# Performance work log

Hardware: AMD Instinct MI355X
Metric: run time of the kernel (lower is better)

## Reference

```python
import jax, jax.numpy as jnp
import numpy as np
from jax import lax

L = 2        # encoder layers
D = 256      # d_model
H = 8        # nhead
DH = D // H  # head dim
CF = 2       # compression_factor (default in CustomizedAttn)
FF = 2048    # dim_feedforward
B = 10       # batch (forced: null_k has shape (10,1,D))
HH = 40
WW = 40
T = HH * WW  # seq len = 1600
EPS = 1e-5


def setup_inputs() -> dict:
    key = jax.random.key(0)
    ks = jax.random.split(key, 16)
    f = lambda k, shp: jax.random.normal(k, shp, jnp.float32) * 0.02
    return {
        "src": jax.random.normal(ks[0], (B, D, HH, WW), jnp.float32),
        "pos_embed": jax.random.normal(ks[1], (B, D, HH, WW), jnp.float32),
        "Wq": f(ks[2], (L, D, D)),
        "Wk": f(ks[3], (L, D, D)),
        "Wv": f(ks[4], (L, D, D)),
        "Wo": f(ks[5], (L, D, D)),
        "bo": jnp.zeros((L, D), jnp.float32),
        "conv_w": f(ks[6], (L, D, D // H, CF)),  # grouped Conv1d weight [out, in/groups, k]
        "conv_b": jnp.zeros((L, D), jnp.float32),
        "null_k": f(ks[7], (L, B, 1, D)),
        "null_v": f(ks[8], (L, B, 1, D)),
        "ln1_g": jnp.ones((L, D), jnp.float32),
        "ln1_b": jnp.zeros((L, D), jnp.float32),
        "ln2_g": jnp.ones((L, D), jnp.float32),
        "ln2_b": jnp.zeros((L, D), jnp.float32),
        "W1": f(ks[9], (L, FF, D)),
        "b1": jnp.zeros((L, FF), jnp.float32),
        "W2": f(ks[10], (L, D, FF)),
        "b2": jnp.zeros((L, D), jnp.float32),
    }


def _layernorm(x, g, b):
    m = jnp.mean(x, axis=-1, keepdims=True)
    v = jnp.var(x, axis=-1, keepdims=True)
    return (x - m) * lax.rsqrt(v + EPS) * g + b


def _attn(x, pos, Wq, Wk, Wv, Wo, bo, cw, cb, nk, nv):
    # x, pos: [B, T, D]
    qk = x + pos
    q = qk @ Wq.T
    k = qk @ Wk.T
    v = x @ Wv.T
    # torch: padding = cf - t % cf -> always in [1, cf], so padding ALWAYS applied
    pad = CF - (T % CF)
    k = jnp.pad(k, ((0, 0), (pad, 0), (0, 0)))
    v = jnp.pad(v, ((0, 0), (pad, 0), (0, 0)))

    def compress(t_):  # grouped strided Conv1d over time, shared weights for k and v
        y = lax.conv_general_dilated(
            t_.transpose(0, 2, 1), cw, (CF,), "VALID",
            dimension_numbers=("NCH", "OIH", "NCH"), feature_group_count=H)
        return (y + cb[None, :, None]).transpose(0, 2, 1)

    k = jnp.concatenate([nk, compress(k)], axis=1)  # [B, Tc+10, D]
    v = jnp.concatenate([nv, compress(v)], axis=1)
    split = lambda t_: t_.reshape(B, t_.shape[1], H, DH).transpose(0, 2, 1, 3)
    qh, kh, vh = split(q), split(k), split(v)
    # NOTE: scale uses FULL d_model (d ** -0.5), faithful to the source.
    dots = jnp.einsum("bhid,bhjd->bhij", qh, kh) * (D ** -0.5)
    # NOTE: the source computes softmax(dots) but then overwrites it with
    # dropout(dots); at inference attention weights are the raw scaled dots.
    out = jnp.einsum("bhij,bhjd->bhid", dots, vh)
    out = out.transpose(0, 2, 1, 3).reshape(B, T, D)
    return out @ Wo.T + bo


def reference(src, pos_embed, Wq, Wk, Wv, Wo, bo, conv_w, conv_b, null_k, null_v,
              ln1_g, ln1_b, ln2_g, ln2_b, W1, b1, W2, b2):
    x = src.reshape(B, D, T).transpose(0, 2, 1)        # [B, T, D]
    pos = pos_embed.reshape(B, D, T).transpose(0, 2, 1)
    for l in range(L):
        a = _attn(x, pos, Wq[l], Wk[l], Wv[l], Wo[l], bo[l],
                  conv_w[l], conv_b[l], null_k[l], null_v[l])
        x = _layernorm(x + a, ln1_g[l], ln1_b[l])
        ff = jnp.maximum(x @ W1[l].T + b1[l], 0.0) @ W2[l].T + b2[l]
        x = _layernorm(x + ff, ln2_g[l], ln2_b[l])
    return x.transpose(0, 2, 1).reshape(B, D, HH, WW)
```

## Files before the change

### kernel.cpp

```cpp
#include <hip/hip_runtime.h>
#include <math.h>

typedef __attribute__((ext_vector_type(8))) short short8;
typedef __attribute__((ext_vector_type(4))) short short4v;
typedef __attribute__((ext_vector_type(4))) float f32x4;
typedef unsigned int u32;

constexpr int Bsz = 10;
constexpr int Dm  = 256;
constexpr int Hh  = 8;
constexpr int Tt  = 1600;
constexpr int FFd = 2048;
constexpr int Tkv = 802;
constexpr int JCH = 8;
constexpr size_t Fsz  = (size_t)Bsz * Tt * Dm;
constexpr size_t PAD  = 65536;
constexpr size_t KVsz = (size_t)Bsz * Tkv * Dm;
constexpr size_t FHsz = (size_t)Bsz * Tt * FFd;
constexpr size_t WBsz = 2621440;

__device__ float g_x[Fsz];
__device__ float g_qk[Fsz];
__device__ float g_t[Fsz];
__device__ float g_kc[KVsz];
__device__ float g_vc[KVsz];
__device__ float g_kvm[(size_t)Bsz * Hh * 32 * 32];
__device__ float g_kvp[(size_t)JCH * Bsz * Hh * 32 * 32];
__device__ float g_pos[Fsz];
__device__ unsigned short g_xb[Fsz + PAD];
__device__ unsigned short g_qkb[Fsz + PAD];
__device__ unsigned short g_tb[Fsz + PAD];
__device__ unsigned short g_qb[Fsz + PAD];
__device__ __attribute__((aligned(16))) unsigned short g_ffh[FHsz + PAD];
__device__ unsigned short g_wb[WBsz];
__device__ unsigned short g_wo2[(size_t)Bsz * Dm * Dm];

__device__ __forceinline__ float* selbuf(int id) {
  switch (id) {
    case 0: return g_x;
    case 1: return g_qk;
    case 2: return g_t;
    case 3: return g_kc;
    case 4: return g_vc;
    case 5: return g_kvm;
    case 6: return (float*)g_ffh;
    default: return (float*)g_ffh + Fsz;
  }
}
__device__ __forceinline__ unsigned short* selbufb(int id) {
  switch (id) {
    case 0: return g_xb;
    case 1: return g_qkb;
    case 2: return g_tb;
    case 3: return g_ffh;
    default: return g_qb;
  }
}

__device__ __forceinline__ unsigned short f2b(float x) {
  unsigned int u = __float_as_uint(x);
  u += 0x7FFFu + ((u >> 16) & 1u);
  return (unsigned short)(u >> 16);
}
__device__ __forceinline__ float b2f(unsigned short u) {
  return __uint_as_float(((unsigned int)u) << 16);
}

__global__ __launch_bounds__(256) void wconv_all_k(
    const float* __restrict__ Wk, const float* __restrict__ Wq,
    const float* __restrict__ Wv, const float* __restrict__ Wo,
    const float* __restrict__ W1, const float* __restrict__ W2) {
  const int i = blockIdx.x * 256 + threadIdx.x;
  float v;
  if (i < 262144) {
    const int l = i >> 17, r = i & 131071;
    v = (r < 65536) ? Wk[l * 65536 + r] : Wq[l * 65536 + (r - 65536)];
  } else if (i < 393216) {
    v = Wv[i - 262144];
  } else if (i < 524288) {
    v = Wo[i - 393216];
  } else if (i < 1572864) {
    v = W1[i - 524288];
  } else {
    v = W2[i - 1572864];
  }
  g_wb[i] = f2b(v);
}

__global__ __launch_bounds__(256) void trans_in2_k(const float* __restrict__ src,
                                                   const float* __restrict__ pose) {
  __shared__ float ts[32][33];
  __shared__ float tp[32][33];
  const int tx = threadIdx.x & 31, ty = threadIdx.x >> 5;
  const int t0 = blockIdx.x * 32, d0 = blockIdx.y * 32, b = blockIdx.z;
  #pragma unroll
  for (int i = ty; i < 32; i += 8) {
    const size_t gi = ((size_t)(b * Dm + d0 + i)) * Tt + t0 + tx;
    ts[i][tx] = src[gi];
    tp[i][tx] = pose[gi];
  }
  __syncthreads();
  #pragma unroll
  for (int i = ty; i < 32; i += 8) {
    const size_t idx = ((size_t)(b * Tt + t0 + i)) * Dm + d0 + tx;
    const float s = ts[tx][i], p = tp[tx][i];
    g_x[idx] = s;
    g_pos[idx] = p;
    g_xb[idx] = f2b(s);
    g_qkb[idx] = f2b(s + p);
  }
}

__global__ __launch_bounds__(256) void trans_out_k(float* out) {
  __shared__ float tile[32][33];
  const int tx = threadIdx.x & 31, ty = threadIdx.x >> 5;
  const int t0 = blockIdx.x * 32, d0 = blockIdx.y * 32, b = blockIdx.z;
  #pragma unroll
  for (int i = ty; i < 32; i += 8)
    tile[i][tx] = g_x[((size_t)(b * Tt + t0 + i)) * Dm + d0 + tx];
  __syncthreads();
  #pragma unroll
  for (int i = ty; i < 32; i += 8)
    out[((size_t)(b * Dm + d0 + i)) * Tt + t0 + tx] = tile[tx][i];
}

template<int BN, bool DUAL, bool PERB, bool RELU, bool BIAS, bool CBF16>
__global__ __launch_bounds__(256) void gemm2_k(
    int Aid, int woff, const float* __restrict__ bias, int Cid, int C2id,
    int NB, int M, int N, int K) {
  constexpr int BM = 128, BK = 64;
  constexpr int ACH = BM * 8;
  constexpr int BCH = BN * 8;
  constexpr int NW = BN / 32;
  __shared__ short8 As8[3][ACH];
  __shared__ short8 Bs8[3][BCH];
  const int tid = threadIdx.x;
  const int lane = tid & 63, wid = tid >> 6;
  const int wr = wid >> 1, wc = wid & 1;

  const int nwg = gridDim.x;
  const int bid = blockIdx.x;
  const int q = nwg >> 3, r = nwg & 7;
  const int xcd = bid & 7, seq = bid >> 3;
  const int wgid = (xcd < r ? xcd * (q + 1) : r * (q + 1) + (xcd - r) * q) + seq;

  int m0, n0, mlim;
  const unsigned short* W16;
  if constexpr (PERB) {
    const int per = 13 * NB;
    const int b = wgid / per;
    const int rem = wgid - b * per;
    m0 = b * Tt + (rem / NB) * BM;
    n0 = (rem % NB) * BN;
    mlim = b * Tt + Tt;
    W16 = g_wo2 + (size_t)b * 65536;
  } else {
    m0 = (wgid / NB) * BM;
    n0 = (wgid % NB) * BN;
    mlim = M;
    W16 = g_wb + woff;
  }

  const unsigned short* A16 = selbufb(Aid);
  const bool second = DUAL && (n0 >= 256);
  float* Cf = selbuf(second ? C2id : Cid);
  unsigned short* C16 = selbufb(second ? C2id : Cid);
  const int gn0 = second ? n0 - 256 : n0;
  const int cstride = DUAL ? 256 : N;

  f32x4 acc[4][NW];
  #pragma unroll
  for (int m = 0; m < 4; ++m)
    #pragma unroll
    for (int n = 0; n < NW; ++n) acc[m][n] = (f32x4){0.f, 0.f, 0.f, 0.f};

  const int lkc = lane >> 4, lrc = lane & 15;

  auto stage = [&](int t, int buf) {
    const int k0 = t * BK;
    #pragma unroll
    for (int i = 0; i < ACH / 256; ++i) {
      const int c = tid + i * 256;
      const int row = c >> 3, kc = c & 7;
      const unsigned short* gs = A16 + (size_t)(m0 + row) * K + k0 +
                                 ((kc ^ (row & 7)) << 3);
      __builtin_amdgcn_global_load_lds(
          (const __attribute__((address_space(1))) u32*)gs,
          (__attribute__((address_space(3))) u32*)&As8[buf][c], 16, 0, 0);
    }
    #pragma unroll
    for (int i = 0; i < BCH / 256; ++i) {
      const int c = tid + i * 256;
      const int row = c >> 3, kc = c & 7;
      const unsigned short* gs = W16 + (size_t)(n0 + row) * K + k0 +
                                 ((kc ^ (row & 7)) << 3);
      __builtin_amdgcn_global_load_lds(
          (const __attribute__((address_space(1))) u32*)gs,
          (__attribute__((address_space(3))) u32*)&Bs8[buf][c], 16, 0, 0);
    }
  };

  const int nt = K / BK;
  stage(0, 0);
  if (nt > 1) stage(1, 1);
  int cur = 0, nxt = 2;
  for (int t = 0; t < nt; ++t) {
    if (t + 1 < nt) {
      asm volatile("s_waitcnt vmcnt(6)" ::: "memory");
    } else {
      asm volatile("s_waitcnt vmcnt(0)" ::: "memory");
    }
    __builtin_amdgcn_sched_barrier(0);
    __builtin_amdgcn_s_barrier();
    __builtin_amdgcn_sched_barrier(0);
    if (t + 2 < nt) stage(t + 2, nxt);
    #pragma unroll
    for (int kk = 0; kk < 2; ++kk) {
      short8 af[4], bf[NW];
      #pragma unroll
      for (int m = 0; m < 4; ++m) {
        const int r2 = wr * 64 + m * 16 + lrc;
        af[m] = As8[cur][r2 * 8 + ((kk * 4 + lkc) ^ (r2 & 7))];
      }
      #pragma unroll
      for (int n = 0; n < NW; ++n) {
        const int cn = wc * (BN / 2) + n * 16 + lrc;
        bf[n] = Bs8[cur][cn * 8 + ((kk * 4 + lkc) ^ (cn & 7))];
      }
      #pragma unroll
      for (int m = 0; m < 4; ++m)
        #pragma unroll
        for (int n = 0; n < NW; ++n)
          acc[m][n] = __builtin_amdgcn_mfma_f32_16x16x32_bf16(
              af[m], bf[n], acc[m][n], 0, 0, 0);
    }
    cur = (cur == 2) ? 0 : cur + 1;
    nxt = (nxt == 2) ? 0 : nxt + 1;
  }

  constexpr int CSTR = (BN == 64) ? BN + 4 : BN;
  float* ldsC = (float*)&As8[0][0];
  {
    asm volatile("s_waitcnt vmcnt(0)" ::: "memory");
    __builtin_amdgcn_s_barrier();
    const int r0 = lkc * 4;
    #pragma unroll
    for (int m = 0; m < 4; ++m)
      #pragma unroll
      for (int n = 0; n < NW; ++n) {
        const int col = wc * (BN / 2) + n * 16 + lrc;
        #pragma unroll
        for (int j = 0; j < 4; ++j)
          ldsC[(wr * 64 + m * 16 + r0 + j) * CSTR + col] = acc[m][n][j];
      }
    __syncthreads();
  }
  if constexpr (CBF16) {
    constexpr int CH = BM * BN / 8;
    #pragma unroll
    for (int i = 0; i < CH / 256; ++i) {
      const int c = tid + i * 256;
      const int rowl = c / (BN / 8), col8 = (c % (BN / 8)) * 8;
      if (PERB && m0 + rowl >= mlim) continue;
      short8 v;
      #pragma unroll
      for (int j = 0; j < 8; ++j) {
        float x = ldsC[rowl * CSTR + col8 + j];
        if (BIAS) x += bias[gn0 + col8 + j];
        if (RELU) x = fmaxf(x, 0.f);
        v[j] = (short)f2b(x);
      }
      *(short8*)(C16 + (size_t)(m0 + rowl) * cstride + gn0 + col8) = v;
    }
  } else {
    constexpr int CH = BM * BN / 4;
    #pragma unroll
    for (int i = 0; i < CH / 256; ++i) {
      const int c = tid + i * 256;
      const int rowl = c / (BN / 4), col4 = (c % (BN / 4)) * 4;
      if (PERB && m0 + rowl >= mlim) continue;
      float4 v;
      float* pv = &v.x;
      #pragma unroll
      for (int j = 0; j < 4; ++j) {
        float x = ldsC[rowl * CSTR + col4 + j];
        if (BIAS) x += bias[gn0 + col4 + j];
        if (RELU) x = fmaxf(x, 0.f);
        pv[j] = x;
      }
      *(float4*)(Cf + (size_t)(m0 + rowl) * cstride + gn0 + col4) = v;
    }
  }
}

__global__ __launch_bounds__(1024, 1) void gemmf_k(
    int Aid, int w1off, int w2off, const float* __restrict__ b1p,
    const float* __restrict__ b2p) {
  constexpr int BM = 128, NCH = 32;
  __shared__ short8 ws[4096];
  __shared__ short8 h8[512];
  __shared__ float b1f[1024];
  const int tid = threadIdx.x;
  const int lane = tid & 63, wid = tid >> 6;
  const int lkc = lane >> 4, lrc = lane & 15;
  const int nwg = gridDim.x, bid = blockIdx.x;
  const int q = nwg >> 3, r = nwg & 7;
  const int xcd = bid & 7, seq = bid >> 3;
  const int wgid = (xcd < r ? xcd * (q + 1) : r * (q + 1) + (xcd - r) * q) + seq;
  const int half = (wgid >= 125) ? 1 : 0;
  const int m0 = (wgid - half * 125) * BM;
  const int hb = half * 1024;
  const unsigned short* A16 = selbufb(Aid);
  const unsigned short* W1p = g_wb + w1off;
  const unsigned short* W2p = g_wb + w2off;
  float* Cf = half ? g_t : g_qk;

  #pragma unroll
  for (int i = 0; i < 4; ++i) {
    const int c = tid + i * 1024;
    const int row = c >> 5, kc = c & 31;
    const unsigned short* gs = A16 + (size_t)(m0 + row) * 256 +
                               ((kc ^ (row & 31)) << 3);
    __builtin_amdgcn_global_load_lds(
        (const __attribute__((address_space(1))) u32*)gs,
        (__attribute__((address_space(3))) u32*)&ws[c], 16, 0, 0);
  }
  __builtin_amdgcn_global_load_lds(
      (const __attribute__((address_space(1))) u32*)(b1p + hb + tid),
      (__attribute__((address_space(3))) u32*)&b1f[tid], 4, 0, 0);
  asm volatile("s_waitcnt vmcnt(0)" ::: "memory");
  __builtin_amdgcn_sched_barrier(0);
  __builtin_amdgcn_s_barrier();

  const int mg = wid >> 1, ng = wid & 1;
  short8 areg[8];
  #pragma unroll
  for (int s = 0; s < 8; ++s) {
    const int r2 = mg * 16 + lrc;
    areg[s] = ws[r2 * 32 + ((s * 4 + lkc) ^ (r2 & 31))];
  }
  asm volatile("s_waitcnt lgkmcnt(0)" ::: "memory");
  __builtin_amdgcn_sched_barrier(0);
  __builtin_amdgcn_s_barrier();

  auto stage_w = [&](int ch, int buf) {
    const int kb = hb + ch * 32;
    {
      const int c = tid;
      const int row = c >> 5, kc = c & 31;
      const unsigned short* gs = W1p + (size_t)(kb + row) * 256 +
                                 ((kc ^ (row & 31)) << 3);
      __builtin_amdgcn_global_load_lds(
          (const __attribute__((address_space(1))) u32*)gs,
          (__attribute__((address_space(3))) u32*)&ws[buf * 2048 + c], 16, 0, 0);
    }
    {
      const int c = tid;
      const int row = c >> 2, kc = c & 3;
      const int g = (kc ^ (row & 3) ^ ((row >> 2) & 3)) & 3;
      const unsigned short* gs = W2p + (size_t)row * 2048 + kb + (g << 3);
      __builtin_amdgcn_global_load_lds(
          (const __attribute__((address_space(1))) u32*)gs,
          (__attribute__((address_space(3))) u32*)&ws[buf * 2048 + 1024 + c],
          16, 0, 0);
    }
  };
  stage_w(0, 0);

  const int wr = wid >> 2, wc = wid & 3;
  f32x4 acc2[2][4];
  #pragma unroll
  for (int m = 0; m < 2; ++m)
    #pragma unroll
    for (int n = 0; n < 4; ++n) acc2[m][n] = (f32x4){0.f, 0.f, 0.f, 0.f};

  for (int ch = 0; ch < NCH; ++ch) {
    const int cur = ch & 1;
    const int wb = cur * 2048;
    asm volatile("s_waitcnt vmcnt(0)" ::: "memory");
    __builtin_amdgcn_sched_barrier(0);
    __builtin_amdgcn_s_barrier();
    __builtin_amdgcn_sched_barrier(0);
    if (ch + 1 < NCH) stage_w(ch + 1, cur ^ 1);

    f32x4 a1 = (f32x4){0.f, 0.f, 0.f, 0.f};
    const int cn1 = ng * 16 + lrc;
    #pragma unroll
    for (int s = 0; s < 8; ++s) {
      short8 bf = ws[wb + cn1 * 32 + ((s * 4 + lkc) ^ cn1)];
      a1 = __builtin_amdgcn_mfma_f32_16x16x32_bf16(areg[s], bf, a1, 0, 0, 0);
    }
    unsigned short* h16 = (unsigned short*)h8;
    #pragma unroll
    for (int j = 0; j < 4; ++j) {
      const int row = mg * 16 + lkc * 4 + j;
      const float v = fmaxf(a1[j] + b1f[ch * 32 + cn1], 0.f);
      const int g = ((cn1 >> 3) ^ (row & 3) ^ ((row >> 2) & 3)) & 3;
      h16[row * 32 + g * 8 + (cn1 & 7)] = f2b(v);
    }
    asm volatile("s_waitcnt lgkmcnt(0)" ::: "memory");
    __builtin_amdgcn_sched_barrier(0);
    __builtin_amdgcn_s_barrier();
    __builtin_amdgcn_sched_barrier(0);

    short8 af2[2], bf2[4];
    #pragma unroll
    for (int m = 0; m < 2; ++m) {
      const int r2 = wr * 32 + m * 16 + lrc;
      af2[m] = h8[r2 * 4 + ((lkc ^ (r2 & 3) ^ ((r2 >> 2) & 3)) & 3)];
    }
    #pragma unroll
    for (int n = 0; n < 4; ++n) {
      const int cn = wc * 64 + n * 16 + lrc;
      bf2[n] = ws[wb + 1024 + cn * 4 + ((lkc ^ (cn & 3) ^ ((cn >> 2) & 3)) & 3)];
    }
    #pragma unroll
    for (int m = 0; m < 2; ++m)
      #pragma unroll
      for (int n = 0; n < 4; ++n)
        acc2[m][n] = __builtin_amdgcn_mfma_f32_16x16x32_bf16(
            af2[m], bf2[n], acc2[m][n], 0, 0, 0);
  }

  const int r0 = lkc * 4;
  #pragma unroll
  for (int m = 0; m < 2; ++m) {
    const int gm = m0 + wr * 32 + m * 16 + r0;
    #pragma unroll
    for (int n = 0; n < 4; ++n) {
      const int gn = wc * 64 + n * 16 + lrc;
      const float bb = (half == 0) ? b2p[gn] : 0.f;
      #pragma unroll
      for (int j = 0; j < 4; ++j)
        Cf[(size_t)(gm + j) * 256 + gn] = acc2[m][n][j] + bb;
    }
  }
}

__global__ __launch_bounds__(256) void compress2_k(
    const float* __restrict__ cw, const float* __restrict__ cb,
    const float* __restrict__ nk, const float* __restrict__ nv) {
  __shared__ float rows[32][256];
  const int tc0 = 1 + blockIdx.x * 16;
  const int b = blockIdx.y;
  const int z = blockIdx.z;
  const int tid = threadIdx.x;
  const int o = tid;
  const int g = o >> 5;

  const unsigned short* srcbuf = z ? g_ffh : g_tb;
  const float* nul = z ? nv : nk;
  float* outb = (z ? g_vc : g_kc) + (size_t)b * Tkv * Dm;

  const int r0g = 2 * tc0 - 2;
  const unsigned short* src = srcbuf + ((size_t)b * Tt + r0g) * Dm;
  #pragma unroll
  for (int i = 0; i < 4; ++i) {
    const int c = tid + i * 256;
    const int row = c >> 5, off = (c & 31) * 8;
    short8 v = *(const short8*)(src + (size_t)row * 256 + off);
    #pragma unroll
    for (int j = 0; j < 8; ++j)
      rows[row][off + j] = b2f((unsigned short)v[j]);
  }

  float we[32], wo[32];
  {
    const float4* wp = (const float4*)(cw + o * 64);
    #pragma unroll
    for (int i = 0; i < 16; ++i) {
      float4 w4 = wp[i];
      we[i * 2 + 0] = w4.x; wo[i * 2 + 0] = w4.y;
      we[i * 2 + 1] = w4.z; wo[i * 2 + 1] = w4.w;
    }
  }
  const float bias = cb[o];
  if (blockIdx.x == 0) {
    outb[o] = nul[b * Dm + o];
    outb[Dm + o] = bias;
  }
  __syncthreads();

  float* outp = outb + o;
  #pragma unroll
  for (int t = 0; t < 16; ++t) {
    const int lr = 2 * t;
    const float* p0 = &rows[lr][g * 32];
    const float* p1 = &rows[lr + 1][g * 32];
    float acc = bias;
    #pragma unroll
    for (int i4 = 0; i4 < 8; ++i4) {
      float4 a0 = *(const float4*)(p0 + i4 * 4);
      float4 a1 = *(const float4*)(p1 + i4 * 4);
      acc = fmaf(we[i4 * 4 + 0], a0.x, acc);
      acc = fmaf(we[i4 * 4 + 1], a0.y, acc);
      acc = fmaf(we[i4 * 4 + 2], a0.z, acc);
      acc = fmaf(we[i4 * 4 + 3], a0.w, acc);
      acc = fmaf(wo[i4 * 4 + 0], a1.x, acc);
      acc = fmaf(wo[i4 * 4 + 1], a1.y, acc);
      acc = fmaf(wo[i4 * 4 + 2], a1.z, acc);
      acc = fmaf(wo[i4 * 4 + 3], a1.w, acc);
    }
    outp[(size_t)(1 + tc0 + t) * Dm] = acc;
  }
}

__global__ __launch_bounds__(256) void kvout1_k() {
  __shared__ float kl[8][32];
  __shared__ float vl[8][32];
  const int bh = blockIdx.x;
  const int js = blockIdx.y;
  const int b = bh >> 3, h = bh & 7;
  const int j0 = js * 101;
  const int jend = (j0 + 101 < Tkv) ? j0 + 101 : Tkv;

  const int tid = threadIdx.x;
  const int lr = tid >> 5;
  const int lc = tid & 31;
  const int e = tid >> 3;
  const int d0 = (tid & 7) * 4;

  float a0 = 0.f, a1 = 0.f, a2 = 0.f, a3 = 0.f;
  const size_t base = (size_t)b * Tkv * Dm + h * 32;

  for (int jc = j0; jc < jend; jc += 8) {
    const int jr = jc + lr;
    if (jr < jend) {
      kl[lr][lc] = g_kc[base + (size_t)jr * Dm + lc];
      vl[lr][lc] = g_vc[base + (size_t)jr * Dm + lc];
    } else {
      kl[lr][lc] = 0.f;
      vl[lr][lc] = 0.f;
    }
    __syncthreads();
    #pragma unroll
    for (int r = 0; r < 8; ++r) {
      const float kf = kl[r][e];
      const float* vr = &vl[r][d0];
      a0 = fmaf(kf, vr[0], a0);
      a1 = fmaf(kf, vr[1], a1);
      a2 = fmaf(kf, vr[2], a2);
      a3 = fmaf(kf, vr[3], a3);
    }
    __syncthreads();
  }
  float* op = g_kvp + ((size_t)js * 80 + bh) * 1024 + e * 32 + d0;
  op[0] = a0; op[1] = a1; op[2] = a2; op[3] = a3;
}

__global__ __launch_bounds__(256) void kvout2_k() {
  const int bh = blockIdx.x;
  const int tid = threadIdx.x;
  const int e = tid >> 3;
  const int d0 = (tid & 7) * 4;
  float a0 = 0.f, a1 = 0.f, a2 = 0.f, a3 = 0.f;
  #pragma unroll
  for (int s = 0; s < JCH; ++s) {
    const float* p = g_kvp + ((size_t)s * 80 + bh) * 1024 + e * 32 + d0;
    a0 += p[0]; a1 += p[1]; a2 += p[2]; a3 += p[3];
  }
  float* op = g_kvm + (size_t)bh * 1024 + e * 32 + d0;
  op[0] = a0 * 0.0625f;
  op[1] = a1 * 0.0625f;
  op[2] = a2 * 0.0625f;
  op[3] = a3 * 0.0625f;
}

__global__ __launch_bounds__(256) void wo2_k(int wooff) {
  const int n = blockIdx.x, b = blockIdx.y;
  const int he = threadIdx.x;
  const int h = he >> 5, e = he & 31;
  const float* kp = g_kvm + ((size_t)(b * Hh + h) * 32 + e) * 32;
  const unsigned short* wp = g_wb + wooff + (size_t)n * Dm + h * 32;
  float acc = 0.f;
  #pragma unroll
  for (int d = 0; d < 32; ++d) acc = fmaf(kp[d], b2f(wp[d]), acc);
  g_wo2[(size_t)b * 65536 + (size_t)n * Dm + he] = f2b(acc);
}

__global__ __launch_bounds__(256) void ln_k(int did, int did2, int did3,
                                            int did4, const float* g,
                                            const float* beta, int do_pos) {
  const int lane = threadIdx.x & 63;
  const int wave = threadIdx.x >> 6;
  const size_t row = (size_t)blockIdx.x * 4 + wave;
  float4 xv = ((const float4*)g_x)[row * 64 + lane];
  float4 dv = ((const float4*)selbuf(did))[row * 64 + lane];
  float v[4] = {xv.x + dv.x, xv.y + dv.y, xv.z + dv.z, xv.w + dv.w};
  if (did2 >= 0) {
    float4 d2 = ((const float4*)selbuf(did2))[row * 64 + lane];
    v[0] += d2.x; v[1] += d2.y; v[2] += d2.z; v[3] += d2.w;
  }
  if (did3 >= 0) {
    float4 d3 = ((const float4*)selbuf(did3))[row * 64 + lane];
    v[0] += d3.x; v[1] += d3.y; v[2] += d3.z; v[3] += d3.w;
  }
  if (did4 >= 0) {
    float4 d4 = ((const float4*)selbuf(did4))[row * 64 + lane];
    v[0] += d4.x; v[1] += d4.y; v[2] += d4.z; v[3] += d4.w;
  }
  float sum = v[0] + v[1] + v[2] + v[3];
  float sq = v[0]*v[0] + v[1]*v[1] + v[2]*v[2] + v[3]*v[3];
  #pragma unroll
  for (int off = 32; off; off >>= 1) {
    sum += __shfl_xor(sum, off);
    sq  += __shfl_xor(sq, off);
  }
  const float mean = sum * (1.f / 256.f);
  const float var = sq * (1.f / 256.f) - mean * mean;
  const float rs = rsqrtf(var + 1e-5f);
  float4 gg = ((const float4*)g)[lane];
  float4 bb = ((const float4*)beta)[lane];
  float4 ov;
  ov.x = (v[0] - mean) * rs * gg.x + bb.x;
  ov.y = (v[1] - mean) * rs * gg.y + bb.y;
  ov.z = (v[2] - mean) * rs * gg.z + bb.z;
  ov.w = (v[3] - mean) * rs * gg.w + bb.w;
  ((float4*)g_x)[row * 64 + lane] = ov;
  short4v sv;
  sv[0] = (short)f2b(ov.x); sv[1] = (short)f2b(ov.y);
  sv[2] = (short)f2b(ov.z); sv[3] = (short)f2b(ov.w);
  *(short4v*)&g_xb[(row * 64 + lane) * 4] = sv;
  if (do_pos) {
    float4 pv = ((const float4*)g_pos)[row * 64 + lane];
    short4v qv;
    qv[0] = (short)f2b(ov.x + pv.x); qv[1] = (short)f2b(ov.y + pv.y);
    qv[2] = (short)f2b(ov.z + pv.z); qv[3] = (short)f2b(ov.w + pv.w);
    *(short4v*)&g_qkb[(row * 64 + lane) * 4] = qv;
  }
}

extern "C" void kernel_launch(void* const* d_in, const int* in_sizes, int n_in,
                              void* d_out, int out_size, void* d_ws, size_t ws_size,
                              hipStream_t stream) {
  const float* src  = (const float*)d_in[0];
  const float* pose = (const float*)d_in[1];
  const float* Wq   = (const float*)d_in[2];
  const float* Wk   = (const float*)d_in[3];
  const float* Wv   = (const float*)d_in[4];
  const float* Wo   = (const float*)d_in[5];
  const float* bo   = (const float*)d_in[6];
  const float* cw   = (const float*)d_in[7];
  const float* cb   = (const float*)d_in[8];
  const float* nk   = (const float*)d_in[9];
  const float* nv   = (const float*)d_in[10];
  const float* ln1g = (const float*)d_in[11];
  const float* ln1b = (const float*)d_in[12];
  const float* ln2g = (const float*)d_in[13];
  const float* ln2b = (const float*)d_in[14];
  const float* W1   = (const float*)d_in[15];
  const float* b1   = (const float*)d_in[16];
  const float* W2   = (const float*)d_in[17];
  const float* b2   = (const float*)d_in[18];

  const int MT = Bsz * Tt;
  const dim3 tgrid(Tt / 32, Dm / 32, Bsz);

  const int OV = 262144, OO = 393216, O1 = 524288, O2 = 1572864;
  wconv_all_k<<<10240, 256, 0, stream>>>(Wk, Wq, Wv, Wo, W1, W2);
  trans_in2_k<<<tgrid, 256, 0, stream>>>(src, pose);

  const int MB = MT / 128;
  for (int l = 0; l < 2; ++l) {
    const float* bo_l = bo + (size_t)l * Dm;
    const float* cw_l = cw + (size_t)l * Dm * 64;
    const float* cb_l = cb + (size_t)l * Dm;
    const float* nk_l = nk + (size_t)l * Bsz * Dm;
    const float* nv_l = nv + (size_t)l * Bsz * Dm;
    const float* b1_l = b1 + (size_t)l * FFd;
    const float* b2_l = b2 + (size_t)l * Dm;
    const int wkq = l * 131072;
    const int wv = OV + l * 65536, wo = OO + l * 65536;
    const int w1 = O1 + l * 524288, w2 = O2 + l * 524288;

    gemm2_k<64, true, false, false, false, true><<<8 * MB, 256, 0, stream>>>(
        1, wkq, nullptr, 2, 4, 8, MT, 512, Dm);
    gemm2_k<64, false, false, false, false, true><<<4 * MB, 256, 0, stream>>>(
        0, wv, nullptr, 3, 3, 4, MT, Dm, Dm);
    compress2_k<<<dim3(50, Bsz, 2), 256, 0, stream>>>(cw_l, cb_l, nk_l, nv_l);
    kvout1_k<<<dim3(Bsz * Hh, JCH), 256, 0, stream>>>();
    kvout2_k<<<Bsz * Hh, 256, 0, stream>>>();
    wo2_k<<<dim3(Dm, Bsz), 256, 0, stream>>>(wo);
    gemm2_k<64, false, true, false, true, false><<<Bsz * 13 * 4, 256, 0, stream>>>(
        4, 0, bo_l, 2, 2, 4, MT, Dm, Dm);
    ln_k<<<MT / 4, 256, 0, stream>>>(2, -1, -1, -1,
                                     ln1g + l * Dm, ln1b + l * Dm, 0);

    gemmf_k<<<250, 1024, 0, stream>>>(0, w1, w2, b1_l, b2_l);
    ln_k<<<MT / 4, 256, 0, stream>>>(1, 2, -1, -1,
                                     ln2g + l * Dm, ln2b + l * Dm,
                                     l == 0 ? 1 : 0);
  }

  trans_out_k<<<tgrid, 256, 0, stream>>>((float*)d_out);
}
```

Measured before the change: 334.1 us.

## Split fused FFN over four hidden quarters with two M-tiles per block

```diff
diff --git a/kernel.cpp b/kernel.cpp
--- a/kernel.cpp
+++ b/kernel.cpp
@@ -296,10 +296,10 @@
 __global__ __launch_bounds__(1024, 1) void gemmf_k(
     int Aid, int w1off, int w2off, const float* __restrict__ b1p,
     const float* __restrict__ b2p) {
-  constexpr int BM = 128, NCH = 32;
+  constexpr int NCH = 16;
   __shared__ short8 ws[4096];
-  __shared__ short8 h8[512];
-  __shared__ float b1f[1024];
+  __shared__ short8 h8[2][512];
+  __shared__ float b1f[512];
   const int tid = threadIdx.x;
   const int lane = tid & 63, wid = tid >> 6;
   const int lkc = lane >> 4, lrc = lane & 15;
@@ -307,37 +307,60 @@
   const int q = nwg >> 3, r = nwg & 7;
   const int xcd = bid & 7, seq = bid >> 3;
   const int wgid = (xcd < r ? xcd * (q + 1) : r * (q + 1) + (xcd - r) * q) + seq;
-  const int half = (wgid >= 125) ? 1 : 0;
-  const int m0 = (wgid - half * 125) * BM;
-  const int hb = half * 1024;
+  const int qd = wgid / 63;
+  const int j  = wgid - qd * 63;
+  const int m0a = (2 * j) * 128;
+  const bool hasB = (2 * j + 1) < 125;
+  const int m0b = hasB ? (2 * j + 1) * 128 : m0a;
+  const int hb = qd * 512;
   const unsigned short* A16 = selbufb(Aid);
   const unsigned short* W1p = g_wb + w1off;
   const unsigned short* W2p = g_wb + w2off;
-  float* Cf = half ? g_t : g_qk;
-
-  #pragma unroll
-  for (int i = 0; i < 4; ++i) {
-    const int c = tid + i * 1024;
-    const int row = c >> 5, kc = c & 31;
-    const unsigned short* gs = A16 + (size_t)(m0 + row) * 256 +
-                               ((kc ^ (row & 31)) << 3);
+  float* Cf;
+  if (qd == 0) Cf = g_qk;
+  else if (qd == 1) Cf = g_t;
+  else Cf = (float*)g_ffh + (size_t)(qd - 2) * Fsz;
+
+  auto stage_a = [&](int m0p) {
+    #pragma unroll
+    for (int i = 0; i < 4; ++i) {
+      const int c = tid + i * 1024;
+      const int row = c >> 5, kc = c & 31;
+      const unsigned short* gs = A16 + (size_t)(m0p + row) * 256 +
+                                 ((kc ^ (row & 31)) << 3);
+      __builtin_amdgcn_global_load_lds(
+          (const __attribute__((address_space(1))) u32*)gs,
+          (__attribute__((address_space(3))) u32*)&ws[c], 16, 0, 0);
+    }
+  };
+  const int mg = wid >> 1, ng = wid & 1;
+  short8 areg0[8], areg1[8];
+
+  stage_a(m0a);
+  if (tid < 512)
     __builtin_amdgcn_global_load_lds(
-        (const __attribute__((address_space(1))) u32*)gs,
-        (__attribute__((address_space(3))) u32*)&ws[c], 16, 0, 0);
-  }
-  __builtin_amdgcn_global_load_lds(
-      (const __attribute__((address_space(1))) u32*)(b1p + hb + tid),
-      (__attribute__((address_space(3))) u32*)&b1f[tid], 4, 0, 0);
+        (const __attribute__((address_space(1))) u32*)(b1p + hb + tid),
+        (__attribute__((address_space(3))) u32*)&b1f[tid], 4, 0, 0);
   asm volatile("s_waitcnt vmcnt(0)" ::: "memory");
   __builtin_amdgcn_sched_barrier(0);
   __builtin_amdgcn_s_barrier();
-
-  const int mg = wid >> 1, ng = wid & 1;
-  short8 areg[8];
   #pragma unroll
   for (int s = 0; s < 8; ++s) {
     const int r2 = mg * 16 + lrc;
-    areg[s] = ws[r2 * 32 + ((s * 4 + lkc) ^ (r2 & 31))];
+    areg0[s] = ws[r2 * 32 + ((s * 4 + lkc) ^ (r2 & 31))];
+  }
+  asm volatile("s_waitcnt lgkmcnt(0)" ::: "memory");
+  __builtin_amdgcn_sched_barrier(0);
+  __builtin_amdgcn_s_barrier();
+
+  stage_a(m0b);
+  asm volatile("s_waitcnt vmcnt(0)" ::: "memory");
+  __builtin_amdgcn_sched_barrier(0);
+  __builtin_amdgcn_s_barrier();
+  #pragma unroll
+  for (int s = 0; s < 8; ++s) {
+    const int r2 = mg * 16 + lrc;
+    areg1[s] = ws[r2 * 32 + ((s * 4 + lkc) ^ (r2 & 31))];
   }
   asm volatile("s_waitcnt lgkmcnt(0)" ::: "memory");
   __builtin_amdgcn_sched_barrier(0);
@@ -368,11 +391,14 @@
   stage_w(0, 0);
 
   const int wr = wid >> 2, wc = wid & 3;
-  f32x4 acc2[2][4];
+  f32x4 acc0[2][4], acc1[2][4];
   #pragma unroll
   for (int m = 0; m < 2; ++m)
     #pragma unroll
-    for (int n = 0; n < 4; ++n) acc2[m][n] = (f32x4){0.f, 0.f, 0.f, 0.f};
+    for (int n = 0; n < 4; ++n) {
+      acc0[m][n] = (f32x4){0.f, 0.f, 0.f, 0.f};
+      acc1[m][n] = (f32x4){0.f, 0.f, 0.f, 0.f};
+    }
 
   for (int ch = 0; ch < NCH; ++ch) {
     const int cur = ch & 1;
@@ -383,56 +409,66 @@
     __builtin_amdgcn_sched_barrier(0);
     if (ch + 1 < NCH) stage_w(ch + 1, cur ^ 1);
 
-    f32x4 a1 = (f32x4){0.f, 0.f, 0.f, 0.f};
+    f32x4 a1a = (f32x4){0.f, 0.f, 0.f, 0.f};
+    f32x4 a1b = (f32x4){0.f, 0.f, 0.f, 0.f};
     const int cn1 = ng * 16 + lrc;
     #pragma unroll
     for (int s = 0; s < 8; ++s) {
       short8 bf = ws[wb + cn1 * 32 + ((s * 4 + lkc) ^ cn1)];
-      a1 = __builtin_amdgcn_mfma_f32_16x16x32_bf16(areg[s], bf, a1, 0, 0, 0);
-    }
-    unsigned short* h16 = (unsigned short*)h8;
-    #pragma unroll
-    for (int j = 0; j < 4; ++j) {
-      const int row = mg * 16 + lkc * 4 + j;
-      const float v = fmaxf(a1[j] + b1f[ch * 32 + cn1], 0.f);
+      a1a = __builtin_amdgcn_mfma_f32_16x16x32_bf16(areg0[s], bf, a1a, 0, 0, 0);
+      a1b = __builtin_amdgcn_mfma_f32_16x16x32_bf16(areg1[s], bf, a1b, 0, 0, 0);
+    }
+    const float bb1 = b1f[ch * 32 + cn1];
+    #pragma unroll
+    for (int j2 = 0; j2 < 4; ++j2) {
+      const int row = mg * 16 + lkc * 4 + j2;
       const int g = ((cn1 >> 3) ^ (row & 3) ^ ((row >> 2) & 3)) & 3;
-      h16[row * 32 + g * 8 + (cn1 & 7)] = f2b(v);
+      ((unsigned short*)h8[0])[row * 32 + g * 8 + (cn1 & 7)] =
+          f2b(fmaxf(a1a[j2] + bb1, 0.f));
+      ((unsigned short*)h8[1])[row * 32 + g * 8 + (cn1 & 7)] =
+          f2b(fmaxf(a1b[j2] + bb1, 0.f));
     }
     asm volatile("s_waitcnt lgkmcnt(0)" ::: "memory");
     __builtin_amdgcn_sched_barrier(0);
     __builtin_amdgcn_s_barrier();
     __builtin_amdgcn_sched_barrier(0);
 
-    short8 af2[2], bf2[4];
-    #pragma unroll
-    for (int m = 0; m < 2; ++m) {
-      const int r2 = wr * 32 + m * 16 + lrc;
-      af2[m] = h8[r2 * 4 + ((lkc ^ (r2 & 3) ^ ((r2 >> 2) & 3)) & 3)];
-    }
+    short8 bf2[4];
     #pragma unroll
     for (int n = 0; n < 4; ++n) {
       const int cn = wc * 64 + n * 16 + lrc;
       bf2[n] = ws[wb + 1024 + cn * 4 + ((lkc ^ (cn & 3) ^ ((cn >> 2) & 3)) & 3)];
     }
     #pragma unroll
-    for (int m = 0; m < 2; ++m)
+    for (int m = 0; m < 2; ++m) {
+      const int r2 = wr * 32 + m * 16 + lrc;
+      const int hi = r2 * 4 + ((lkc ^ (r2 & 3) ^ ((r2 >> 2) & 3)) & 3);
+      short8 af0 = h8[0][hi];
+      short8 af1 = h8[1][hi];
       #pragma unroll
-      for (int n = 0; n < 4; ++n)
-        acc2[m][n] = __builtin_amdgcn_mfma_f32_16x16x32_bf16(
-            af2[m], bf2[n], acc2[m][n], 0, 0, 0);
+      for (int n = 0; n < 4; ++n) {
+        acc0[m][n] = __builtin_amdgcn_mfma_f32_16x16x32_bf16(
+            af0, bf2[n], acc0[m][n], 0, 0, 0);
+        acc1[m][n] = __builtin_amdgcn_mfma_f32_16x16x32_bf16(
+            af1, bf2[n], acc1[m][n], 0, 0, 0);
+      }
+    }
   }
 
   const int r0 = lkc * 4;
   #pragma unroll
   for (int m = 0; m < 2; ++m) {
-    const int gm = m0 + wr * 32 + m * 16 + r0;
     #pragma unroll
     for (int n = 0; n < 4; ++n) {
       const int gn = wc * 64 + n * 16 + lrc;
-      const float bb = (half == 0) ? b2p[gn] : 0.f;
+      const float bb = (qd == 0) ? b2p[gn] : 0.f;
       #pragma unroll
-      for (int j = 0; j < 4; ++j)
-        Cf[(size_t)(gm + j) * 256 + gn] = acc2[m][n][j] + bb;
+      for (int j2 = 0; j2 < 4; ++j2) {
+        const int gr = wr * 32 + m * 16 + r0 + j2;
+        Cf[(size_t)(m0a + gr) * 256 + gn] = acc0[m][n][j2] + bb;
+        if (hasB)
+          Cf[(size_t)(m0b + gr) * 256 + gn] = acc1[m][n][j2] + bb;
+      }
     }
   }
 }
@@ -686,8 +722,8 @@
     ln_k<<<MT / 4, 256, 0, stream>>>(2, -1, -1, -1,
                                      ln1g + l * Dm, ln1b + l * Dm, 0);
 
-    gemmf_k<<<250, 1024, 0, stream>>>(0, w1, w2, b1_l, b2_l);
-    ln_k<<<MT / 4, 256, 0, stream>>>(1, 2, -1, -1,
+    gemmf_k<<<252, 1024, 0, stream>>>(0, w1, w2, b1_l, b2_l);
+    ln_k<<<MT / 4, 256, 0, stream>>>(1, 2, 6, 7,
                                      ln2g + l * Dm, ln2b + l * Dm,
                                      l == 0 ? 1 : 0);
   }
```

New measurement: 528.3 us. +58.1%, slower.
